# Performance work log

Hardware: AMD Instinct MI355X
Metric: run time of the kernel (lower is better)

## Reference

```python
import jax, jax.numpy as jnp
import numpy as np

N = 10000
IN_DIM = 256
HID = 256
HEADS = 8
NUM_CLASSES = 40
EPS = 1e-5
NEG_SLOPE = 0.2


def gat_conv(x, src, dst, W, a_src, a_dst, bias, concat):
    # x: [N, F_in]; W: [F_in, H*C]; a_src/a_dst: [H, C]
    n = x.shape[0]
    H, C = a_src.shape
    h = (x @ W).reshape(n, H, C)                       # [N,H,C]
    s_src = jnp.einsum('nhc,hc->nh', h, a_src)         # [N,H]
    s_dst = jnp.einsum('nhc,hc->nh', h, a_dst)         # [N,H]
    score = jax.nn.leaky_relu(s_src[src] + s_dst[dst], NEG_SLOPE)  # [E,H]
    m = jax.lax.stop_gradient(jax.ops.segment_max(score, dst, num_segments=n))
    e = jnp.exp(score - m[dst])                        # [E,H]
    denom = jax.ops.segment_sum(e, dst, num_segments=n)
    alpha = e / denom[dst]                             # per-dst edge softmax
    msg = h[src] * alpha[:, :, None]                   # [E,H,C]
    out = jax.ops.segment_sum(msg, dst, num_segments=n)  # [N,H,C]
    out = out.reshape(n, H * C) if concat else out.mean(axis=1)
    return out + bias


def batch_norm(x, gamma, beta):
    mu = x.mean(axis=0)
    var = x.var(axis=0)
    return gamma * (x - mu) * jax.lax.rsqrt(var + EPS) + beta


def setup_inputs() -> dict:
    key = jax.random.key(0)
    ks = jax.random.split(key, 16)
    C0 = HID // HEADS  # 32, concat layer
    x = jax.random.normal(ks[0], (N, IN_DIM), jnp.float32)
    edge_index = jax.random.randint(ks[1], (2, 160000), 0, N, jnp.int32)
    def lin(k, fi, fo):
        return jax.random.normal(k, (fi, fo), jnp.float32) / np.sqrt(fi)
    return {
        'x': x,
        'edge_index': edge_index,
        'W0': lin(ks[2], IN_DIM, HEADS * C0),
        'a_src0': jax.random.normal(ks[3], (HEADS, C0), jnp.float32) * 0.1,
        'a_dst0': jax.random.normal(ks[4], (HEADS, C0), jnp.float32) * 0.1,
        'b0': jnp.zeros((HID,), jnp.float32),
        'g0': jnp.ones((HID,), jnp.float32),
        'be0': jnp.zeros((HID,), jnp.float32),
        'W1': lin(ks[5], HID, HEADS * HID),
        'a_src1': jax.random.normal(ks[6], (HEADS, HID), jnp.float32) * 0.1,
        'a_dst1': jax.random.normal(ks[7], (HEADS, HID), jnp.float32) * 0.1,
        'b1': jnp.zeros((HID,), jnp.float32),
        'g1': jnp.ones((HID,), jnp.float32),
        'be1': jnp.zeros((HID,), jnp.float32),
        'Wc': lin(ks[8], HID, NUM_CLASSES),
        'bc': jnp.zeros((NUM_CLASSES,), jnp.float32),
    }


def reference(x, edge_index, W0, a_src0, a_dst0, b0, g0, be0,
              W1, a_src1, a_dst1, b1, g1, be1, Wc, bc):
    n = x.shape[0]
    loops = jnp.arange(n, dtype=edge_index.dtype)
    src = jnp.concatenate([edge_index[0], loops])  # add_self_loops=True
    dst = jnp.concatenate([edge_index[1], loops])

    # layer 0: concat=True -> [N, 256]
    h = gat_conv(x, src, dst, W0, a_src0, a_dst0, b0, concat=True)
    h = jax.nn.elu(batch_norm(h, g0, be0))
    # i==0: no residual; dropout is identity at eval

    # layer 1 (last): concat=False (mean over heads) -> [N, 256]
    h_in = h
    h = gat_conv(h, src, dst, W1, a_src1, a_dst1, b1, concat=False)
    h = jax.nn.elu(batch_norm(h, g1, be1)) + h_in  # residual for i>0

    return h @ Wc + bc  # logits [N, num_classes]
```

## Files before the change

### kernel.cpp

```cpp
#include <hip/hip_runtime.h>
#include <math.h>

#define NN 10000
#define HEADS 8
#define NCLS 40
#define CHK 64
#define LOG2E 1.4426950408889634f

typedef __attribute__((ext_vector_type(8))) short short8;
typedef __attribute__((ext_vector_type(8))) unsigned short ushort8v;
typedef __attribute__((ext_vector_type(4))) float floatx4;

static __device__ __forceinline__ short f2bf(float f) {
    unsigned u = __builtin_bit_cast(unsigned, f);
    unsigned r = (u + 0x7fff + ((u >> 16) & 1)) >> 16;
    return (short)r;
}
static __device__ __forceinline__ float bf2f(unsigned short u) {
    unsigned x = ((unsigned)u) << 16;
    return __builtin_bit_cast(float, x);
}
static __device__ __forceinline__ void gl2lds16(const void* g, void* l) {
    __builtin_amdgcn_global_load_lds(
        (const __attribute__((address_space(1))) unsigned int*)g,
        (__attribute__((address_space(3))) unsigned int*)l, 16, 0, 0);
}

__global__ __launch_bounds__(512) void gemm_bf16_w256(
    const short* __restrict__ A, const short* __restrict__ Bt,
    float* __restrict__ C, short* __restrict__ Cbf,
    float* __restrict__ stats,
    const float* __restrict__ asrc, const float* __restrict__ adst,
    float* __restrict__ s0,
    const int* __restrict__ esrc, const int* __restrict__ edst,
    int* __restrict__ cursor, int* __restrict__ elist, int E, int scatBlocks,
    const float* __restrict__ W1, const float* __restrict__ a_src1,
    const float* __restrict__ a_dst1, float* __restrict__ v1,
    short* __restrict__ W1pT,
    int gemmBlocks, int M, int K, float alpha)
{
    __shared__ short As[2][64 * 64];
    __shared__ short Bs[2][256 * 64];
    const int tid = threadIdx.x;
    if ((int)blockIdx.x >= gemmBlocks) {
        int td = (int)blockIdx.x - gemmBlocks;
        if (td < scatBlocks) {
            int e = td * 512 + tid;
            if (e < E) {
                int dn = edst[e];
                int pos = atomicAdd(&cursor[dn], 1);
                elist[pos] = esrc[e];
            }
            return;
        }
        td -= scatBlocks;
        if (td < 8) {
            int idx = td * 512 + tid;
            int f = idx >> 4, j = idx & 15;
            int h = j & 7;
            const float* a = (j < 8) ? a_src1 : a_dst1;
            float s = 0.f;
            for (int c = 0; c < 256; c++)
                s += W1[f * 2048 + h * 256 + c] * a[h * 256 + c];
            v1[idx] = s;
            return;
        }
        td -= 8;
        {
            float (*tile)[33] = (float(*)[33])&As[0][0];
            int h = td >> 6, f0 = ((td >> 3) & 7) * 32, c0 = (td & 7) * 32;
            int tx = tid & 31, ty = tid >> 5;
            for (int r = ty; r < 32; r += 16)
                tile[r][tx] = W1[(size_t)(f0 + r) * 2048 + h * 256 + c0 + tx];
            __syncthreads();
            for (int r = ty; r < 32; r += 16)
                W1pT[(size_t)(c0 + r) * 2048 + h * 256 + f0 + tx] = f2bf(tile[tx][r]);
            return;
        }
    }
    const int w = tid >> 6, L = tid & 63;
    const int quad = L >> 4, lr = L & 15;
    const int row0 = blockIdx.x * 64;

    const int schunk = (L & 7) ^ (L >> 3);
    const int sarow = w * 8 + (L >> 3);
    int ga = row0 + sarow; if (ga > M - 1) ga = M - 1;
    const short* agp = A + (size_t)ga * K + schunk * 8;
    const int sbrow = w * 32 + (L >> 3);
    const short* bgp0 = Bt + (size_t)(sbrow +  0) * K + schunk * 8;
    const short* bgp1 = Bt + (size_t)(sbrow +  8) * K + schunk * 8;
    const short* bgp2 = Bt + (size_t)(sbrow + 16) * K + schunk * 8;
    const short* bgp3 = Bt + (size_t)(sbrow + 24) * K + schunk * 8;

    floatx4 acc[4][2];
    const floatx4 zf = {0.f, 0.f, 0.f, 0.f};
    #pragma unroll
    for (int i = 0; i < 4; i++)
        #pragma unroll
        for (int j = 0; j < 2; j++) acc[i][j] = zf;

    const int nt = K >> 6;
    {
        gl2lds16(agp,  &As[0][w * 512]);
        gl2lds16(bgp0, &Bs[0][w * 2048]);
        gl2lds16(bgp1, &Bs[0][w * 2048 + 512]);
        gl2lds16(bgp2, &Bs[0][w * 2048 + 1024]);
        gl2lds16(bgp3, &Bs[0][w * 2048 + 1536]);
    }
    __syncthreads();
    int cur = 0;
    for (int t = 0; t < nt; t++) {
        if (t + 1 < nt) {
            const int k0 = (t + 1) << 6;
            const int nb = cur ^ 1;
            gl2lds16(agp + k0,  &As[nb][w * 512]);
            gl2lds16(bgp0 + k0, &Bs[nb][w * 2048]);
            gl2lds16(bgp1 + k0, &Bs[nb][w * 2048 + 512]);
            gl2lds16(bgp2 + k0, &Bs[nb][w * 2048 + 1024]);
            gl2lds16(bgp3 + k0, &Bs[nb][w * 2048 + 1536]);
        }
        #pragma unroll
        for (int ks = 0; ks < 2; ks++) {
            const int sl = ((ks * 4 + quad) ^ (lr & 7)) * 8;
            short8 bfr[2];
            #pragma unroll
            for (int j = 0; j < 2; j++)
                bfr[j] = *(const short8*)&Bs[cur][(w * 32 + j * 16 + lr) * 64 + sl];
            #pragma unroll
            for (int i = 0; i < 4; i++) {
                short8 afr = *(const short8*)&As[cur][(i * 16 + lr) * 64 + sl];
                #pragma unroll
                for (int j = 0; j < 2; j++)
                    acc[i][j] = __builtin_amdgcn_mfma_f32_16x16x32_bf16(afr, bfr[j], acc[i][j], 0, 0, 0);
            }
        }
        __syncthreads();
        cur ^= 1;
    }
    float s[2] = {0.f, 0.f}, s2[2] = {0.f, 0.f};
    #pragma unroll
    for (int j = 0; j < 2; j++) {
        int ccol = w * 32 + j * 16 + lr;
        #pragma unroll
        for (int i = 0; i < 4; i++) {
            #pragma unroll
            for (int r = 0; r < 4; r++) {
                int crow = row0 + i * 16 + quad * 4 + r;
                if (crow < M) {
                    float v = alpha * acc[i][j][r];
                    if (C)   C[(size_t)crow * 256 + ccol] = v;
                    if (Cbf) Cbf[(size_t)crow * 256 + ccol] = f2bf(v);
                    s[j] += v; s2[j] += v * v;
                }
            }
        }
    }
    if (stats) {
        #pragma unroll
        for (int j = 0; j < 2; j++) {
            s[j]  += __shfl_xor(s[j], 16, 64);  s[j]  += __shfl_xor(s[j], 32, 64);
            s2[j] += __shfl_xor(s2[j], 16, 64); s2[j] += __shfl_xor(s2[j], 32, 64);
        }
        if (L < 16) {
            #pragma unroll
            for (int j = 0; j < 2; j++) {
                int ccol = w * 32 + j * 16 + L;
                atomicAdd(&stats[ccol], s[j]);
                atomicAdd(&stats[256 + ccol], s2[j]);
            }
        }
    }
    if (s0) {
        float as0 = asrc[w * 32 + lr];
        float as1 = asrc[w * 32 + 16 + lr];
        float ad0 = adst[w * 32 + lr];
        float ad1 = adst[w * 32 + 16 + lr];
        #pragma unroll
        for (int i = 0; i < 4; i++) {
            #pragma unroll
            for (int r = 0; r < 4; r++) {
                float ps = acc[i][0][r] * as0 + acc[i][1][r] * as1;
                float pd = acc[i][0][r] * ad0 + acc[i][1][r] * ad1;
                #pragma unroll
                for (int off = 1; off < 16; off <<= 1) {
                    ps += __shfl_xor(ps, off, 64);
                    pd += __shfl_xor(pd, off, 64);
                }
                if (lr == 0) {
                    int crow = row0 + i * 16 + quad * 4 + r;
                    if (crow < M) {
                        s0[crow * 16 + w] = alpha * ps;
                        s0[crow * 16 + 8 + w] = alpha * pd;
                    }
                }
            }
        }
    }
}

__global__ __launch_bounds__(256) void classifier_fused(
    const float* __restrict__ X, const float* __restrict__ stats,
    const float* __restrict__ g, const float* __restrict__ be,
    const unsigned short* __restrict__ resid,
    const short* __restrict__ Bt, float* __restrict__ C,
    const float* __restrict__ bias, int M, int Nn, int K)
{
    __shared__ short As[2][32 * 64];
    __shared__ short Bs[2][64 * 64];
    const int tid = threadIdx.x;
    const int w = tid >> 6, L = tid & 63;
    const int quad = L >> 4, lr = L & 15;
    const int row0 = blockIdx.x * 32;

    const int schunk = (L & 7) ^ (L >> 3);
    int ga = row0 + w * 8 + (L >> 3); if (ga > M - 1) ga = M - 1;
    int gbrow = w * 16 + (L >> 3);
    int gb0 = gbrow;     if (gb0 > Nn - 1) gb0 = Nn - 1;
    int gb1 = gbrow + 8; if (gb1 > Nn - 1) gb1 = Nn - 1;
    const float* xg = X + (size_t)ga * K + schunk * 8;
    const unsigned short* rg = resid + (size_t)ga * K + schunk * 8;
    const short* bgp0 = Bt + (size_t)gb0 * K + schunk * 8;
    const short* bgp1 = Bt + (size_t)gb1 * K + schunk * 8;

    floatx4 acc[2];
    const floatx4 zf = {0.f, 0.f, 0.f, 0.f};
    acc[0] = zf; acc[1] = zf;
    const float invN = 1.0f / NN;
    const int nt = K >> 6;

    floatx4 xa, xb2; ushort8v rv;
    xa  = *(const floatx4*)(xg);
    xb2 = *(const floatx4*)(xg + 4);
    rv  = *(const ushort8v*)(rg);
    gl2lds16(bgp0, &Bs[0][w * 1024]);
    gl2lds16(bgp1, &Bs[0][w * 1024 + 512]);
    {
        const int c = schunk * 8;
        short8 av;
        #pragma unroll
        for (int q = 0; q < 8; q++) {
            float m  = stats[c + q] * invN;
            float sq = stats[256 + c + q] * invN;
            float rs = rsqrtf(sq - m * m + 1e-5f) * g[c + q];
            float sh = be[c + q] - m * rs;
            float v = (q < 4 ? xa[q & 3] : xb2[q & 3]) * rs + sh;
            v = (v > 0.f) ? v : (expf(v) - 1.f);
            v += bf2f(rv[q]);
            av[q] = f2bf(v);
        }
        *(short8*)&As[0][w * 512 + L * 8] = av;
    }
    __syncthreads();
    int cur = 0;
    for (int t = 0; t < nt; t++) {
        floatx4 nxa, nxb2; ushort8v nrv;
        if (t + 1 < nt) {
            const int k0 = (t + 1) << 6;
            nxa  = *(const floatx4*)(xg + k0);
            nxb2 = *(const floatx4*)(xg + k0 + 4);
            nrv  = *(const ushort8v*)(rg + k0);
            gl2lds16(bgp0 + k0, &Bs[cur ^ 1][w * 1024]);
            gl2lds16(bgp1 + k0, &Bs[cur ^ 1][w * 1024 + 512]);
        }
        #pragma unroll
        for (int ks = 0; ks < 2; ks++) {
            const int sl = ((ks * 4 + quad) ^ (lr & 7)) * 8;
            short8 bfr = *(const short8*)&Bs[cur][(w * 16 + lr) * 64 + sl];
            #pragma unroll
            for (int i = 0; i < 2; i++) {
                short8 afr = *(const short8*)&As[cur][(i * 16 + lr) * 64 + sl];
                acc[i] = __builtin_amdgcn_mfma_f32_16x16x32_bf16(afr, bfr, acc[i], 0, 0, 0);
            }
        }
        if (t + 1 < nt) {
            const int c = schunk * 8 + ((t + 1) << 6);
            short8 av;
            #pragma unroll
            for (int q = 0; q < 8; q++) {
                float m  = stats[c + q] * invN;
                float sq = stats[256 + c + q] * invN;
                float rs = rsqrtf(sq - m * m + 1e-5f) * g[c + q];
                float sh = be[c + q] - m * rs;
                float v = (q < 4 ? nxa[q & 3] : nxb2[q & 3]) * rs + sh;
                v = (v > 0.f) ? v : (expf(v) - 1.f);
                v += bf2f(nrv[q]);
                av[q] = f2bf(v);
            }
            *(short8*)&As[cur ^ 1][w * 512 + L * 8] = av;
        }
        __syncthreads();
        cur ^= 1;
    }
    const int ccol = w * 16 + lr;
    if (ccol < Nn) {
        float bv = bias ? bias[ccol] : 0.f;
        #pragma unroll
        for (int i = 0; i < 2; i++) {
            #pragma unroll
            for (int r = 0; r < 4; r++) {
                int crow = row0 + i * 16 + quad * 4 + r;
                if (crow < M) C[(size_t)crow * Nn + ccol] = acc[i][r] + bv;
            }
        }
    }
}

__global__ __launch_bounds__(256) void prep_a(
    const float* __restrict__ x, const float* __restrict__ W0,
    const float* __restrict__ Wc, const int* __restrict__ edst, int E,
    short* __restrict__ xb, short* __restrict__ W0T, short* __restrict__ WcT,
    int* __restrict__ counts)
{
    const int b = blockIdx.x, t = threadIdx.x;
    if (b < 2500) {
        int i = b * 256 + t;
        floatx4 v = ((const floatx4*)x)[i];
        short4 o = {f2bf(v[0]), f2bf(v[1]), f2bf(v[2]), f2bf(v[3])};
        ((short4*)xb)[i] = o;
    } else if (b < 2756) {
        int o = b - 2500;
        W0T[o * 256 + t] = f2bf(W0[t * 256 + o]);
    } else if (b < 2796) {
        int o = b - 2756;
        WcT[o * 256 + t] = f2bf(Wc[t * 40 + o]);
    } else {
        int e = (b - 2796) * 256 + t;
        if (e < E) atomicAdd(&counts[edst[e]], 1);
    }
}

__global__ __launch_bounds__(256) void scan_kernel(
    int* __restrict__ counts, int* __restrict__ offsets,
    int* __restrict__ cursor, int* __restrict__ elist, int n)
{
    __shared__ int wsum[4];
    const int t = threadIdx.x;
    const int P = (n + 255) >> 8;
    const int lane = t & 63, wid = t >> 6;
    const int base = t * P;
    int s = 0;
    for (int j = 0; j < P; j++) {
        int i = base + j;
        if (i < n) s += counts[i] + 1;
    }
    int inc = s;
    #pragma unroll
    for (int off = 1; off < 64; off <<= 1) {
        int tv = __shfl_up(inc, off, 64);
        if (lane >= off) inc += tv;
    }
    if (lane == 63) wsum[wid] = inc;
    __syncthreads();
    int wo = 0;
    #pragma unroll
    for (int k2 = 0; k2 < 4; k2++) {
        int v = wsum[k2];
        if (k2 < wid) wo += v;
    }
    int run = wo + inc - s;
    for (int j = 0; j < P; j++) {
        int i = base + j;
        if (i < n) {
            int d2 = counts[i] + 1;
            counts[i] = d2;
            offsets[i] = run;
            elist[run] = i;
            cursor[i] = run + 1;
            run += d2;
        }
    }
}

__global__ __launch_bounds__(256) void agg0_fused(
    const unsigned short* __restrict__ h0b, const float* __restrict__ s0,
    const int* __restrict__ offsets, const int* __restrict__ counts,
    const int* __restrict__ elist, float* __restrict__ out)
{
    __shared__ float pw_s[4][CHK * 8];
    __shared__ int   sn_s[4][CHK];
    const int wid = threadIdx.x >> 6, L = threadIdx.x & 63;
    const int n = blockIdx.x * 4 + wid;
    float* pw = pw_s[wid];
    int*   sw = sn_s[wid];
    const int deg = counts[n], start = offsets[n];
    const int hL = L >> 3;

    floatx4 sda = *(const floatx4*)(s0 + n * 16 + 8);
    floatx4 sdb = *(const floatx4*)(s0 + n * 16 + 12);
    float sd[8] = {sda[0], sda[1], sda[2], sda[3], sdb[0], sdb[1], sdb[2], sdb[3]};
    float lp[8] = {0.f, 0.f, 0.f, 0.f, 0.f, 0.f, 0.f, 0.f};
    float a0 = 0.f, a1 = 0.f, a2 = 0.f, a3 = 0.f;

    for (int e0 = 0; e0 < deg; e0 += CHK) {
        int ch = deg - e0; if (ch > CHK) ch = CHK;
        if (L < ch) {
            int sn = elist[start + e0 + L];
            sw[L] = sn;
            floatx4 ssa = *(const floatx4*)(s0 + sn * 16);
            floatx4 ssb = *(const floatx4*)(s0 + sn * 16 + 4);
            float ss[8] = {ssa[0], ssa[1], ssa[2], ssa[3], ssb[0], ssb[1], ssb[2], ssb[3]};
            float p[8];
            #pragma unroll
            for (int h = 0; h < 8; h++) {
                float v = ss[h] + sd[h];
                v = (v > 0.f) ? v : 0.2f * v;
                p[h] = exp2f(v * LOG2E);
                lp[h] += p[h];
            }
            floatx4 p0 = {p[0], p[1], p[2], p[3]};
            floatx4 p1 = {p[4], p[5], p[6], p[7]};
            *(floatx4*)&pw[L * 8] = p0;
            *(floatx4*)&pw[L * 8 + 4] = p1;
        }
        int e = 0;
        for (; e + 2 <= ch; e += 2) {
            float wA = pw[e * 8 + hL];
            float wB = pw[e * 8 + 8 + hL];
            ushort4 vA = *(const ushort4*)(h0b + (size_t)sw[e] * 256 + 4 * L);
            ushort4 vB = *(const ushort4*)(h0b + (size_t)sw[e + 1] * 256 + 4 * L);
            a0 += wA * bf2f(vA.x); a1 += wA * bf2f(vA.y);
            a2 += wA * bf2f(vA.z); a3 += wA * bf2f(vA.w);
            a0 += wB * bf2f(vB.x); a1 += wB * bf2f(vB.y);
            a2 += wB * bf2f(vB.z); a3 += wB * bf2f(vB.w);
        }
        if (e < ch) {
            float wA = pw[e * 8 + hL];
            ushort4 vA = *(const ushort4*)(h0b + (size_t)sw[e] * 256 + 4 * L);
            a0 += wA * bf2f(vA.x); a1 += wA * bf2f(vA.y);
            a2 += wA * bf2f(vA.z); a3 += wA * bf2f(vA.w);
        }
    }
    #pragma unroll
    for (int off = 1; off < 64; off <<= 1)
        #pragma unroll
        for (int h = 0; h < 8; h++)
            lp[h] += __shfl_xor(lp[h], off, 64);
    float inv = 1.f / lp[hL];
    floatx4 o = {a0 * inv, a1 * inv, a2 * inv, a3 * inv};
    *(floatx4*)(out + (size_t)n * 256 + 4 * L) = o;
}

__global__ __launch_bounds__(256) void agg1_full(
    const unsigned short* __restrict__ hb, const float* __restrict__ s1,
    const int* __restrict__ offsets, const int* __restrict__ counts,
    const int* __restrict__ elist, short* __restrict__ aggout)
{
    __shared__ float pw_s[4][CHK * 8];
    __shared__ int   sn_s[4][CHK];
    const int wid = threadIdx.x >> 6, L = threadIdx.x & 63;
    const int n = blockIdx.x * 4 + wid;
    float* pw = pw_s[wid];
    int*   sw = sn_s[wid];
    const int deg = counts[n], start = offsets[n];

    floatx4 sda = *(const floatx4*)(s1 + n * 16 + 8);
    floatx4 sdb = *(const floatx4*)(s1 + n * 16 + 12);
    float sd[8] = {sda[0], sda[1], sda[2], sda[3], sdb[0], sdb[1], sdb[2], sdb[3]};
    float lp[8] = {0.f, 0.f, 0.f, 0.f, 0.f, 0.f, 0.f, 0.f};
    float acc[8][4];
    #pragma unroll
    for (int h = 0; h < 8; h++)
        #pragma unroll
        for (int f = 0; f < 4; f++) acc[h][f] = 0.f;

    for (int e0 = 0; e0 < deg; e0 += CHK) {
        int ch = deg - e0; if (ch > CHK) ch = CHK;
        if (L < ch) {
            int sn = elist[start + e0 + L];
            sw[L] = sn;
            floatx4 ssa = *(const floatx4*)(s1 + sn * 16);
            floatx4 ssb = *(const floatx4*)(s1 + sn * 16 + 4);
            float ss[8] = {ssa[0], ssa[1], ssa[2], ssa[3], ssb[0], ssb[1], ssb[2], ssb[3]};
            float p[8];
            #pragma unroll
            for (int h = 0; h < 8; h++) {
                float v = ss[h] + sd[h];
                v = (v > 0.f) ? v : 0.2f * v;
                p[h] = exp2f(v * LOG2E);
                lp[h] += p[h];
            }
            floatx4 p0 = {p[0], p[1], p[2], p[3]};
            floatx4 p1 = {p[4], p[5], p[6], p[7]};
            *(floatx4*)&pw[L * 8] = p0;
            *(floatx4*)&pw[L * 8 + 4] = p1;
        }
        int e = 0;
        for (; e + 2 <= ch; e += 2) {
            floatx4 p0A = *(const floatx4*)&pw[e * 8];
            floatx4 p1A = *(const floatx4*)&pw[e * 8 + 4];
            floatx4 p0B = *(const floatx4*)&pw[e * 8 + 8];
            floatx4 p1B = *(const floatx4*)&pw[e * 8 + 12];
            ushort4 vA = *(const ushort4*)(hb + (size_t)sw[e] * 256 + 4 * L);
            ushort4 vB = *(const ushort4*)(hb + (size_t)sw[e + 1] * 256 + 4 * L);
            float a0 = bf2f(vA.x), a1 = bf2f(vA.y), a2 = bf2f(vA.z), a3 = bf2f(vA.w);
            float b0 = bf2f(vB.x), b1 = bf2f(vB.y), b2 = bf2f(vB.z), b3 = bf2f(vB.w);
            #pragma unroll
            for (int h = 0; h < 4; h++) {
                acc[h][0] += p0A[h] * a0;     acc[h][1] += p0A[h] * a1;
                acc[h][2] += p0A[h] * a2;     acc[h][3] += p0A[h] * a3;
                acc[h + 4][0] += p1A[h] * a0; acc[h + 4][1] += p1A[h] * a1;
                acc[h + 4][2] += p1A[h] * a2; acc[h + 4][3] += p1A[h] * a3;
            }
            #pragma unroll
            for (int h = 0; h < 4; h++) {
                acc[h][0] += p0B[h] * b0;     acc[h][1] += p0B[h] * b1;
                acc[h][2] += p0B[h] * b2;     acc[h][3] += p0B[h] * b3;
                acc[h + 4][0] += p1B[h] * b0; acc[h + 4][1] += p1B[h] * b1;
                acc[h + 4][2] += p1B[h] * b2; acc[h + 4][3] += p1B[h] * b3;
            }
        }
        if (e < ch) {
            floatx4 p0A = *(const floatx4*)&pw[e * 8];
            floatx4 p1A = *(const floatx4*)&pw[e * 8 + 4];
            ushort4 vA = *(const ushort4*)(hb + (size_t)sw[e] * 256 + 4 * L);
            float a0 = bf2f(vA.x), a1 = bf2f(vA.y), a2 = bf2f(vA.z), a3 = bf2f(vA.w);
            #pragma unroll
            for (int h = 0; h < 4; h++) {
                acc[h][0] += p0A[h] * a0;     acc[h][1] += p0A[h] * a1;
                acc[h][2] += p0A[h] * a2;     acc[h][3] += p0A[h] * a3;
                acc[h + 4][0] += p1A[h] * a0; acc[h + 4][1] += p1A[h] * a1;
                acc[h + 4][2] += p1A[h] * a2; acc[h + 4][3] += p1A[h] * a3;
            }
        }
    }
    #pragma unroll
    for (int off = 1; off < 64; off <<= 1)
        #pragma unroll
        for (int h = 0; h < 8; h++)
            lp[h] += __shfl_xor(lp[h], off, 64);
    #pragma unroll
    for (int h = 0; h < 8; h++) {
        float inv = 1.f / lp[h];
        short4 o = {f2bf(acc[h][0] * inv), f2bf(acc[h][1] * inv),
                    f2bf(acc[h][2] * inv), f2bf(acc[h][3] * inv)};
        *(short4*)(aggout + (size_t)n * 2048 + h * 256 + 4 * L) = o;
    }
}

__global__ __launch_bounds__(1024) void bn_stats_kernel(
    const float* __restrict__ x, float* __restrict__ stats, int n)
{
    __shared__ float red[16][512];
    const int t = threadIdx.x;
    const int sub = t >> 6, c4 = (t & 63) * 4;
    floatx4 s = {0.f, 0.f, 0.f, 0.f}, s2 = {0.f, 0.f, 0.f, 0.f};
    for (int r = blockIdx.x * 16 + sub; r < n; r += gridDim.x * 16) {
        floatx4 v = *(const floatx4*)(x + (size_t)r * 256 + c4);
        s += v; s2 += v * v;
    }
    #pragma unroll
    for (int k = 0; k < 4; k++) {
        red[sub][c4 + k] = s[k];
        red[sub][256 + c4 + k] = s2[k];
    }
    __syncthreads();
    if (t < 512) {
        float acc = 0.f;
        #pragma unroll
        for (int i = 0; i < 16; i++) acc += red[i][t];
        atomicAdd(&stats[t], acc);
    }
}

__global__ __launch_bounds__(256) void bnapply_score1(
    const float* __restrict__ xg, const float* __restrict__ stats,
    const float* __restrict__ g, const float* __restrict__ be,
    const float* __restrict__ v1, short* __restrict__ hactb, float* __restrict__ s1)
{
    __shared__ float row[256];
    __shared__ float part[16][17];
    const int n = blockIdx.x, t = threadIdx.x;
    const float invN = 1.0f / NN;
    float mu = stats[t] * invN;
    float var = stats[256 + t] * invN - mu * mu;
    float v = g[t] * (xg[(size_t)n * 256 + t] - mu) * rsqrtf(var + 1e-5f) + be[t];
    v = (v > 0.f) ? v : (expf(v) - 1.f);
    hactb[(size_t)n * 256 + t] = f2bf(v);
    row[t] = v;
    __syncthreads();
    int j = t & 15, f0 = t >> 4;
    float p = 0.f;
    #pragma unroll
    for (int k = 0; k < 16; k++)
        p += row[f0 * 16 + k] * v1[(f0 * 16 + k) * 16 + j];
    part[f0][j] = p;
    __syncthreads();
    if (t < 16) {
        float s = 0.f;
        #pragma unroll
        for (int k = 0; k < 16; k++) s += part[k][t];
        s1[n * 16 + t] = s;
    }
}

extern "C" void kernel_launch(void* const* d_in, const int* in_sizes, int n_in,
                              void* d_out, int out_size, void* d_ws, size_t ws_size,
                              hipStream_t stream) {
    const float* x      = (const float*)d_in[0];
    const int*   eidx   = (const int*)d_in[1];
    const float* W0     = (const float*)d_in[2];
    const float* a_src0 = (const float*)d_in[3];
    const float* a_dst0 = (const float*)d_in[4];
    const float* g0     = (const float*)d_in[6];
    const float* be0    = (const float*)d_in[7];
    const float* W1     = (const float*)d_in[8];
    const float* a_src1 = (const float*)d_in[9];
    const float* a_dst1 = (const float*)d_in[10];
    const float* g1     = (const float*)d_in[12];
    const float* be1    = (const float*)d_in[13];
    const float* Wc     = (const float*)d_in[14];
    const float* bc     = (const float*)d_in[15];
    float* out = (float*)d_out;

    const int E = in_sizes[1] / 2;
    const int* esrc = eidx;
    const int* edst = eidx + E;

    char* ws = (char*)d_ws;
    size_t off = 0;
    auto alloc = [&](size_t bytes) {
        void* p = ws + off;
        off += (bytes + 255) & ~(size_t)255;
        return p;
    };
    float* stats   = (float*)alloc(1024 * 4);
    int*   counts  = (int*)alloc(NN * 4);
    float* out1    = (float*)alloc((size_t)NN * 256 * 4);
    short* h0b     = (short*)alloc((size_t)NN * 256 * 2);
    short* xb      = (short*)alloc((size_t)NN * 256 * 2);
    float* s0      = (float*)alloc((size_t)NN * 16 * 4);
    float* s1      = (float*)alloc((size_t)NN * 16 * 4);
    float* v1      = (float*)alloc(4096 * 4);
    float* h_gat0  = (float*)alloc((size_t)NN * 256 * 4);
    short* hactb   = (short*)alloc((size_t)NN * 256 * 2);
    short* agg1bf  = (short*)alloc((size_t)NN * 2048 * 2);
    short* W0T     = (short*)alloc((size_t)256 * 256 * 2);
    short* W1pT    = (short*)alloc((size_t)256 * 2048 * 2);
    short* WcT     = (short*)alloc((size_t)64 * 256 * 2);
    int* offsets   = (int*)alloc((NN + 16) * 4);
    int* cursor    = (int*)alloc(NN * 4);
    int* elist     = (int*)alloc((size_t)(E + NN) * 4);

    float* stats0 = stats;
    float* stats1 = stats + 512;

    hipMemsetAsync(stats, 0, 1024 * 4 + NN * 4, stream);

    const int cntBlocks = (E + 255) / 256;
    const int scat512   = (E + 511) / 512;

    prep_a<<<2796 + cntBlocks, 256, 0, stream>>>(
        x, W0, Wc, edst, E, xb, W0T, WcT, counts);

    scan_kernel<<<1, 256, 0, stream>>>(counts, offsets, cursor, elist, NN);

    const int gy = (NN + 63) / 64;

    gemm_bf16_w256<<<gy + scat512 + 8 + 512, 512, 0, stream>>>(
        xb, W0T, nullptr, h0b, nullptr,
        a_src0, a_dst0, s0,
        esrc, edst, cursor, elist, E, scat512,
        W1, a_src1, a_dst1, v1, W1pT,
        gy, NN, 256, 1.0f);

    agg0_fused<<<NN / 4, 256, 0, stream>>>(
        (const unsigned short*)h0b, s0, offsets, counts, elist, h_gat0);
    bn_stats_kernel<<<64, 1024, 0, stream>>>(h_gat0, stats0, NN);
    bnapply_score1<<<NN, 256, 0, stream>>>(h_gat0, stats0, g0, be0, v1, hactb, s1);

    agg1_full<<<NN / 4, 256, 0, stream>>>(
        (const unsigned short*)hactb, s1, offsets, counts, elist, agg1bf);
    gemm_bf16_w256<<<gy, 512, 0, stream>>>(
        agg1bf, W1pT, out1, nullptr, stats1,
        nullptr, nullptr, nullptr,
        nullptr, nullptr, nullptr, nullptr, 0, 0,
        nullptr, nullptr, nullptr, nullptr, nullptr,
        gy, NN, 2048, 0.125f);

    classifier_fused<<<(NN + 31) / 32, 256, 0, stream>>>(
        out1, stats1, g1, be1, (const unsigned short*)hactb,
        WcT, out, bc, NN, NCLS, 256);
}
```

Before: 288.2 us.

## Split GEMM into 64x128 tiles with grouped block order and widen scan

New measurement: 248.3 us. 13.8% less time.

```diff
diff --git a/kernel.cpp b/kernel.cpp
--- a/kernel.cpp
+++ b/kernel.cpp
@@ -26,7 +26,7 @@
         (__attribute__((address_space(3))) unsigned int*)l, 16, 0, 0);
 }
 
-__global__ __launch_bounds__(512) void gemm_bf16_w256(
+__global__ __launch_bounds__(256) void gemm_bf16_w128(
     const short* __restrict__ A, const short* __restrict__ Bt,
     float* __restrict__ C, short* __restrict__ Cbf,
     float* __restrict__ stats,
@@ -37,15 +37,16 @@
     const float* __restrict__ W1, const float* __restrict__ a_src1,
     const float* __restrict__ a_dst1, float* __restrict__ v1,
     short* __restrict__ W1pT,
-    int gemmBlocks, int M, int K, float alpha)
+    int gemmBlocks, int gridY,
+    int M, int Nn, int K, float alpha)
 {
     __shared__ short As[2][64 * 64];
-    __shared__ short Bs[2][256 * 64];
+    __shared__ short Bs[2][128 * 64];
     const int tid = threadIdx.x;
     if ((int)blockIdx.x >= gemmBlocks) {
         int td = (int)blockIdx.x - gemmBlocks;
         if (td < scatBlocks) {
-            int e = td * 512 + tid;
+            int e = td * 256 + tid;
             if (e < E) {
                 int dn = edst[e];
                 int pos = atomicAdd(&cursor[dn], 1);
@@ -54,8 +55,8 @@
             return;
         }
         td -= scatBlocks;
-        if (td < 8) {
-            int idx = td * 512 + tid;
+        if (td < 16) {
+            int idx = td * 256 + tid;
             int f = idx >> 4, j = idx & 15;
             int h = j & 7;
             const float* a = (j < 8) ? a_src1 : a_dst1;
@@ -65,32 +66,44 @@
             v1[idx] = s;
             return;
         }
-        td -= 8;
+        td -= 16;
         {
             float (*tile)[33] = (float(*)[33])&As[0][0];
             int h = td >> 6, f0 = ((td >> 3) & 7) * 32, c0 = (td & 7) * 32;
             int tx = tid & 31, ty = tid >> 5;
-            for (int r = ty; r < 32; r += 16)
+            for (int r = ty; r < 32; r += 8)
                 tile[r][tx] = W1[(size_t)(f0 + r) * 2048 + h * 256 + c0 + tx];
             __syncthreads();
-            for (int r = ty; r < 32; r += 16)
+            for (int r = ty; r < 32; r += 8)
                 W1pT[(size_t)(c0 + r) * 2048 + h * 256 + f0 + tx] = f2bf(tile[tx][r]);
             return;
         }
     }
     const int w = tid >> 6, L = tid & 63;
     const int quad = L >> 4, lr = L & 15;
-    const int row0 = blockIdx.x * 64;
+    const int d = blockIdx.x;
+    const int by = (d >> 4) * 8 + (d & 7);
+    const int bx = (d >> 3) & 1;
+    if (by >= gridY) return;
+    const int col0 = bx * 128, row0 = by * 64;
 
     const int schunk = (L & 7) ^ (L >> 3);
-    const int sarow = w * 8 + (L >> 3);
-    int ga = row0 + sarow; if (ga > M - 1) ga = M - 1;
-    const short* agp = A + (size_t)ga * K + schunk * 8;
+    const int sarow = w * 16 + (L >> 3);
+    int ga0 = row0 + sarow;     if (ga0 > M - 1) ga0 = M - 1;
+    int ga1 = row0 + sarow + 8; if (ga1 > M - 1) ga1 = M - 1;
+    const short* agp0 = A + (size_t)ga0 * K + schunk * 8;
+    const short* agp1 = A + (size_t)ga1 * K + schunk * 8;
     const int sbrow = w * 32 + (L >> 3);
-    const short* bgp0 = Bt + (size_t)(sbrow +  0) * K + schunk * 8;
-    const short* bgp1 = Bt + (size_t)(sbrow +  8) * K + schunk * 8;
-    const short* bgp2 = Bt + (size_t)(sbrow + 16) * K + schunk * 8;
-    const short* bgp3 = Bt + (size_t)(sbrow + 24) * K + schunk * 8;
+    int gb[4];
+    #pragma unroll
+    for (int c = 0; c < 4; c++) {
+        gb[c] = col0 + sbrow + c * 8;
+        if (gb[c] > Nn - 1) gb[c] = Nn - 1;
+    }
+    const short* bgp0 = Bt + (size_t)gb[0] * K + schunk * 8;
+    const short* bgp1 = Bt + (size_t)gb[1] * K + schunk * 8;
+    const short* bgp2 = Bt + (size_t)gb[2] * K + schunk * 8;
+    const short* bgp3 = Bt + (size_t)gb[3] * K + schunk * 8;
 
     floatx4 acc[4][2];
     const floatx4 zf = {0.f, 0.f, 0.f, 0.f};
@@ -100,20 +113,20 @@
         for (int j = 0; j < 2; j++) acc[i][j] = zf;
 
     const int nt = K >> 6;
-    {
-        gl2lds16(agp,  &As[0][w * 512]);
-        gl2lds16(bgp0, &Bs[0][w * 2048]);
-        gl2lds16(bgp1, &Bs[0][w * 2048 + 512]);
-        gl2lds16(bgp2, &Bs[0][w * 2048 + 1024]);
-        gl2lds16(bgp3, &Bs[0][w * 2048 + 1536]);
-    }
+    gl2lds16(agp0, &As[0][w * 1024]);
+    gl2lds16(agp1, &As[0][w * 1024 + 512]);
+    gl2lds16(bgp0, &Bs[0][w * 2048]);
+    gl2lds16(bgp1, &Bs[0][w * 2048 + 512]);
+    gl2lds16(bgp2, &Bs[0][w * 2048 + 1024]);
+    gl2lds16(bgp3, &Bs[0][w * 2048 + 1536]);
     __syncthreads();
     int cur = 0;
     for (int t = 0; t < nt; t++) {
         if (t + 1 < nt) {
             const int k0 = (t + 1) << 6;
             const int nb = cur ^ 1;
-            gl2lds16(agp + k0,  &As[nb][w * 512]);
+            gl2lds16(agp0 + k0, &As[nb][w * 1024]);
+            gl2lds16(agp1 + k0, &As[nb][w * 1024 + 512]);
             gl2lds16(bgp0 + k0, &Bs[nb][w * 2048]);
             gl2lds16(bgp1 + k0, &Bs[nb][w * 2048 + 512]);
             gl2lds16(bgp2 + k0, &Bs[nb][w * 2048 + 1024]);
@@ -140,7 +153,8 @@
     float s[2] = {0.f, 0.f}, s2[2] = {0.f, 0.f};
     #pragma unroll
     for (int j = 0; j < 2; j++) {
-        int ccol = w * 32 + j * 16 + lr;
+        int ccol = col0 + w * 32 + j * 16 + lr;
+        if (ccol >= Nn) continue;
         #pragma unroll
         for (int i = 0; i < 4; i++) {
             #pragma unroll
@@ -148,8 +162,8 @@
                 int crow = row0 + i * 16 + quad * 4 + r;
                 if (crow < M) {
                     float v = alpha * acc[i][j][r];
-                    if (C)   C[(size_t)crow * 256 + ccol] = v;
-                    if (Cbf) Cbf[(size_t)crow * 256 + ccol] = f2bf(v);
+                    if (C)   C[(size_t)crow * Nn + ccol] = v;
+                    if (Cbf) Cbf[(size_t)crow * Nn + ccol] = f2bf(v);
                     s[j] += v; s2[j] += v * v;
                 }
             }
@@ -164,17 +178,20 @@
         if (L < 16) {
             #pragma unroll
             for (int j = 0; j < 2; j++) {
-                int ccol = w * 32 + j * 16 + L;
-                atomicAdd(&stats[ccol], s[j]);
-                atomicAdd(&stats[256 + ccol], s2[j]);
+                int ccol = col0 + w * 32 + j * 16 + L;
+                if (ccol < Nn) {
+                    atomicAdd(&stats[ccol], s[j]);
+                    atomicAdd(&stats[256 + ccol], s2[j]);
+                }
             }
         }
     }
     if (s0) {
-        float as0 = asrc[w * 32 + lr];
-        float as1 = asrc[w * 32 + 16 + lr];
-        float ad0 = adst[w * 32 + lr];
-        float ad1 = adst[w * 32 + 16 + lr];
+        const int head = bx * 4 + w;
+        float as0 = asrc[col0 + w * 32 + lr];
+        float as1 = asrc[col0 + w * 32 + 16 + lr];
+        float ad0 = adst[col0 + w * 32 + lr];
+        float ad1 = adst[col0 + w * 32 + 16 + lr];
         #pragma unroll
         for (int i = 0; i < 4; i++) {
             #pragma unroll
@@ -189,8 +206,8 @@
                 if (lr == 0) {
                     int crow = row0 + i * 16 + quad * 4 + r;
                     if (crow < M) {
-                        s0[crow * 16 + w] = alpha * ps;
-                        s0[crow * 16 + 8 + w] = alpha * pd;
+                        s0[crow * 16 + head] = alpha * ps;
+                        s0[crow * 16 + 8 + head] = alpha * pd;
                     }
                 }
             }
@@ -329,19 +346,22 @@
     }
 }
 
-__global__ __launch_bounds__(256) void scan_kernel(
+__global__ __launch_bounds__(1024) void scan_kernel(
     int* __restrict__ counts, int* __restrict__ offsets,
-    int* __restrict__ cursor, int* __restrict__ elist, int n)
+    int* __restrict__ cursor, int* __restrict__ elist)
 {
-    __shared__ int wsum[4];
-    const int t = threadIdx.x;
-    const int P = (n + 255) >> 8;
-    const int lane = t & 63, wid = t >> 6;
+    __shared__ int wsum[16];
+    const int t = threadIdx.x, lane = t & 63, wid = t >> 6;
+    constexpr int P = 10;
     const int base = t * P;
+    int deg[P], loc[P];
     int s = 0;
+    #pragma unroll
     for (int j = 0; j < P; j++) {
         int i = base + j;
-        if (i < n) s += counts[i] + 1;
+        loc[j] = s;
+        deg[j] = (i < NN) ? counts[i] + 1 : 0;
+        s += deg[j];
     }
     int inc = s;
     #pragma unroll
@@ -351,22 +371,27 @@
     }
     if (lane == 63) wsum[wid] = inc;
     __syncthreads();
-    int wo = 0;
-    #pragma unroll
-    for (int k2 = 0; k2 < 4; k2++) {
-        int v = wsum[k2];
-        if (k2 < wid) wo += v;
-    }
-    int run = wo + inc - s;
+    if (t < 16) {
+        int v = wsum[t];
+        int winc = v;
+        #pragma unroll
+        for (int off = 1; off < 16; off <<= 1) {
+            int tv = __shfl_up(winc, off, 16);
+            if (t >= off) winc += tv;
+        }
+        wsum[t] = winc - v;
+    }
+    __syncthreads();
+    int excl = inc - s + wsum[wid];
+    #pragma unroll
     for (int j = 0; j < P; j++) {
         int i = base + j;
-        if (i < n) {
-            int d2 = counts[i] + 1;
-            counts[i] = d2;
-            offsets[i] = run;
-            elist[run] = i;
-            cursor[i] = run + 1;
-            run += d2;
+        if (i < NN) {
+            int o = excl + loc[j];
+            counts[i] = deg[j];
+            offsets[i] = o;
+            elist[o] = i;
+            cursor[i] = o + 1;
         }
     }
 }
@@ -647,21 +672,21 @@
     hipMemsetAsync(stats, 0, 1024 * 4 + NN * 4, stream);
 
     const int cntBlocks = (E + 255) / 256;
-    const int scat512   = (E + 511) / 512;
 
     prep_a<<<2796 + cntBlocks, 256, 0, stream>>>(
         x, W0, Wc, edst, E, xb, W0T, WcT, counts);
 
-    scan_kernel<<<1, 256, 0, stream>>>(counts, offsets, cursor, elist, NN);
+    scan_kernel<<<1, 1024, 0, stream>>>(counts, offsets, cursor, elist);
 
     const int gy = (NN + 63) / 64;
-
-    gemm_bf16_w256<<<gy + scat512 + 8 + 512, 512, 0, stream>>>(
+    const int gB = 16 * ((gy + 7) / 8);
+
+    gemm_bf16_w128<<<gB + cntBlocks + 528, 256, 0, stream>>>(
         xb, W0T, nullptr, h0b, nullptr,
         a_src0, a_dst0, s0,
-        esrc, edst, cursor, elist, E, scat512,
+        esrc, edst, cursor, elist, E, cntBlocks,
         W1, a_src1, a_dst1, v1, W1pT,
-        gy, NN, 256, 1.0f);
+        gB, gy, NN, 256, 256, 1.0f);
 
     agg0_fused<<<NN / 4, 256, 0, stream>>>(
         (const unsigned short*)h0b, s0, offsets, counts, elist, h_gat0);
@@ -670,12 +695,12 @@
 
     agg1_full<<<NN / 4, 256, 0, stream>>>(
         (const unsigned short*)hactb, s1, offsets, counts, elist, agg1bf);
-    gemm_bf16_w256<<<gy, 512, 0, stream>>>(
+    gemm_bf16_w128<<<gB, 256, 0, stream>>>(
         agg1bf, W1pT, out1, nullptr, stats1,
         nullptr, nullptr, nullptr,
         nullptr, nullptr, nullptr, nullptr, 0, 0,
         nullptr, nullptr, nullptr, nullptr, nullptr,
-        gy, NN, 2048, 0.125f);
+        gB, gy, NN, 256, 2048, 0.125f);
 
     classifier_fused<<<(NN + 31) / 32, 256, 0, stream>>>(
         out1, stats1, g1, be1, (const unsigned short*)hactb,
```
